# Performance work log

Measured on AMD Instinct MI355X. Metric: run time of the kernel, lower is better.

The kernel has to match this reference:

```python
import jax, jax.numpy as jnp
import numpy as np

B, N_E, E_DIM = 131072, 1024, 64
BETA = 0.25


def setup_inputs() -> dict:
    key = jax.random.key(0)
    kz, kw = jax.random.split(key)
    z = jax.random.normal(kz, (B, E_DIM), dtype=jnp.float32)
    # nn.Embedding init: uniform(-1/n_e, 1/n_e)
    emb_w = jax.random.uniform(kw, (N_E, E_DIM), dtype=jnp.float32,
                               minval=-1.0 / N_E, maxval=1.0 / N_E)
    return {"z": z, "emb_w": emb_w}


def reference(z, emb_w):
    beta = jnp.float32(BETA)
    # pairwise squared distances: [B, n_e]
    d = (jnp.sum(z * z, axis=1, keepdims=True)
         + jnp.sum(emb_w * emb_w, axis=1)
         - 2.0 * jnp.einsum('bd,nd->bn', z, emb_w))
    idx = jnp.argmin(d, axis=1)                      # [B]
    z_q = jnp.take(emb_w, idx, axis=0)               # [B, e_dim]
    # legacy=False branch
    loss = (beta * jnp.mean((jax.lax.stop_gradient(z_q) - z) ** 2)
            + jnp.mean((z_q - jax.lax.stop_gradient(z)) ** 2))
    # straight-through estimator
    z_q_st = z + jax.lax.stop_gradient(z_q - z)
    # torch.var is unbiased (ddof=1)
    v = jnp.var(idx.astype(jnp.float32), ddof=1)
    return (z_q_st, loss, idx, v)
```

## Files before the change

kernel.cpp:

```cpp
#include <hip/hip_runtime.h>
#include <stdint.h>


typedef __attribute__((ext_vector_type(8))) __bf16 bf16x8;
typedef __attribute__((ext_vector_type(4))) float f32x4;

#define OUT_LOSS 8388608
#define OUT_IDX  8388609
#define OUT_VAR  8519681

#define WS_LOSS  0
#define WS_S1    4096
#define WS_S2    8192
#define WS_EFRAG 12288
#define WS_EE    143360

__device__ __forceinline__ void gld_lds16(const void* g, void* l) {
  __builtin_amdgcn_global_load_lds(
      (const __attribute__((address_space(1))) unsigned*)g,
      (__attribute__((address_space(3))) unsigned*)l, 16, 0, 0);
}

__global__ void vq_prep(const float* __restrict__ emb, char* __restrict__ ws) {
  bf16x8* efrag = (bf16x8*)(ws + WS_EFRAG);
  float* eeoff = (float*)(ws + WS_EE);
  const int t = blockIdx.x;
  const int l = threadIdx.x;
  const int n = t * 16 + (l & 15);
  const int kb0 = (l >> 4) * 8;
  const float* er = emb + n * 64;
  for (int j = 0; j < 2; ++j) {
    const int kb = j * 32 + kb0;
    bf16x8 h;
#pragma unroll
    for (int i = 0; i < 8; ++i) h[i] = (__bf16)(-2.0f * er[kb + i]);
    efrag[(t * 2 + j) * 64 + l] = h;
  }
  if (l < 16) {
    const float* e2 = emb + (t * 16 + l) * 64;
    float s = 0.f;
#pragma unroll
    for (int d = 0; d < 64; ++d) s += e2[d] * e2[d];
    eeoff[t * 16 + l] = s + 0.875f;
  }
}

__global__ void __launch_bounds__(512) vq_main(
    const float* __restrict__ z, const float* __restrict__ emb,
    float* __restrict__ out, char* __restrict__ ws) {
  __shared__ char smfrag[3][16384];
  __shared__ float see[1024];
  __shared__ float sL[8];
  __shared__ int sA[8], sB[8];

  const int tid = threadIdx.x;
  const int wave = tid >> 6, lane = tid & 63;
  const int lr = lane & 15, ksl = lane >> 4;
  const int k0 = ksl * 8;
  const int row_base = blockIdx.x * 256 + wave * 32;

#define STAGE(ph, buf)                                                          \
  {                                                                             \
    _Pragma("unroll")                                                           \
    for (int i_ = 0; i_ < 2; ++i_)                                              \
      gld_lds16(ws + WS_EFRAG + (ph) * 16384 + wave * 2048 + i_ * 1024 + lane * 16, \
                smfrag[buf] + wave * 2048 + i_ * 1024);                         \
  }

  const float* zra = z + (size_t)(row_base + lr) * 64;
  const float* zrb = z + (size_t)(row_base + 16 + lr) * 64;
  f32x4 a0 = *(const f32x4*)(zra + k0);
  f32x4 a1 = *(const f32x4*)(zra + k0 + 4);
  f32x4 a2 = *(const f32x4*)(zra + 32 + k0);
  f32x4 a3 = *(const f32x4*)(zra + 32 + k0 + 4);
  f32x4 b0 = *(const f32x4*)(zrb + k0);
  f32x4 b1 = *(const f32x4*)(zrb + k0 + 4);
  f32x4 b2 = *(const f32x4*)(zrb + 32 + k0);
  f32x4 b3 = *(const f32x4*)(zrb + 32 + k0 + 4);

  if (wave < 4)
    gld_lds16(ws + WS_EE + wave * 1024 + lane * 16, (char*)see + wave * 1024);
  STAGE(0, 0);
  STAGE(1, 1);

  bf16x8 zfa0, zfa1, zfb0, zfb1;
  float zza, zzb;
  {
    float sa = 0.f, sb = 0.f;
#pragma unroll
    for (int i = 0; i < 4; ++i) {
      zfa0[i] = (__bf16)a0[i]; zfa0[4 + i] = (__bf16)a1[i];
      zfa1[i] = (__bf16)a2[i]; zfa1[4 + i] = (__bf16)a3[i];
      zfb0[i] = (__bf16)b0[i]; zfb0[4 + i] = (__bf16)b1[i];
      zfb1[i] = (__bf16)b2[i]; zfb1[4 + i] = (__bf16)b3[i];
      sa += a0[i] * a0[i] + a1[i] * a1[i] + a2[i] * a2[i] + a3[i] * a3[i];
      sb += b0[i] * b0[i] + b1[i] * b1[i] + b2[i] * b2[i] + b3[i] * b3[i];
    }
    sa += __shfl_xor(sa, 16, 64); sa += __shfl_xor(sa, 32, 64);
    sb += __shfl_xor(sb, 16, 64); sb += __shfl_xor(sb, 32, 64);
    zza = sa; zzb = sb;
  }

  unsigned rka = 0xFFFFFFFFu, rkb = 0xFFFFFFFFu;
  const unsigned kj0 = (unsigned)(ksl * 4), kj1 = kj0 + 1, kj2 = kj0 + 2, kj3 = kj0 + 3;

  for (int ph = 0; ph < 8; ++ph) {
    if (ph < 7) { asm volatile("s_waitcnt vmcnt(2)" ::: "memory"); }
    else        { asm volatile("s_waitcnt vmcnt(0)" ::: "memory"); }
    __builtin_amdgcn_sched_barrier(0);
    __builtin_amdgcn_s_barrier();
    if (ph < 6) STAGE(ph + 2, (ph + 2) % 3);
    const bf16x8* sfrag = (const bf16x8*)(smfrag[ph % 3]);
    __builtin_amdgcn_s_setprio(1);
#pragma unroll
    for (int tt = 0; tt < 8; ++tt) {
      const int g = ph * 8 + tt;
      bf16x8 e0 = sfrag[(tt * 2 + 0) * 64 + lane];
      bf16x8 e1 = sfrag[(tt * 2 + 1) * 64 + lane];
      const f32x4 ee = *(const f32x4*)(see + g * 16 + ksl * 4);
      f32x4 a = __builtin_amdgcn_mfma_f32_16x16x32_bf16(e0, zfa0, ee, 0, 0, 0);
      a = __builtin_amdgcn_mfma_f32_16x16x32_bf16(e1, zfa1, a, 0, 0, 0);
      f32x4 b = __builtin_amdgcn_mfma_f32_16x16x32_bf16(e0, zfb0, ee, 0, 0, 0);
      b = __builtin_amdgcn_mfma_f32_16x16x32_bf16(e1, zfb1, b, 0, 0, 0);
      const unsigned g16 = (unsigned)(g * 16);
      {
        const unsigned q0 = (__float_as_uint(a[0]) << 10) + kj0;
        const unsigned q1 = (__float_as_uint(a[1]) << 10) + kj1;
        const unsigned q2 = (__float_as_uint(a[2]) << 10) + kj2;
        const unsigned q3 = (__float_as_uint(a[3]) << 10) + kj3;
        rka = min(rka, min(min(q0, q1), min(q2, q3)) + g16);
      }
      {
        const unsigned q0 = (__float_as_uint(b[0]) << 10) + kj0;
        const unsigned q1 = (__float_as_uint(b[1]) << 10) + kj1;
        const unsigned q2 = (__float_as_uint(b[2]) << 10) + kj2;
        const unsigned q3 = (__float_as_uint(b[3]) << 10) + kj3;
        rkb = min(rkb, min(min(q0, q1), min(q2, q3)) + g16);
      }
    }
    __builtin_amdgcn_s_setprio(0);
  }
#undef STAGE

  rka = min(rka, (unsigned)__shfl_xor((int)rka, 16, 64));
  rka = min(rka, (unsigned)__shfl_xor((int)rka, 32, 64));
  rkb = min(rkb, (unsigned)__shfl_xor((int)rkb, 16, 64));
  rkb = min(rkb, (unsigned)__shfl_xor((int)rkb, 32, 64));

  const int erow = lane >> 1, eseg = lane & 1;
  const int src = erow & 15;
  const unsigned ka = (unsigned)__shfl((int)rka, src, 64);
  const unsigned kb = (unsigned)__shfl((int)rkb, src, 64);
  const float za = __shfl(zza, src, 64);
  const float zb = __shfl(zzb, src, 64);
  const unsigned k = (erow < 16) ? ka : kb;
  const float zzv = (erow < 16) ? za : zb;
  const unsigned idx = k & 1023u;
  const size_t rowg = (size_t)row_base + erow;
  const f32x4* ep = (const f32x4*)(emb + (size_t)idx * 64 + eseg * 32);
  f32x4* op = (f32x4*)(out + rowg * 64 + eseg * 32);
#pragma unroll
  for (int c = 0; c < 8; ++c) op[c] = ep[c];

  float ls = 0.f; int s1 = 0, s2 = 0;
  if (eseg == 0) {
    ls = zzv + __uint_as_float(0x3F400000u | (k >> 10)) - 0.875f;
    s1 = (int)idx;
    s2 = (int)(idx * idx);
    out[OUT_IDX + rowg] = (float)idx;
  }
#pragma unroll
  for (int off = 1; off < 64; off <<= 1) {
    ls += __shfl_xor(ls, off, 64);
    s1 += __shfl_xor(s1, off, 64);
    s2 += __shfl_xor(s2, off, 64);
  }
  if (lane == 0) { sL[wave] = ls; sA[wave] = s1; sB[wave] = s2; }
  __syncthreads();
  if (tid == 0) {
    float L = 0; int a = 0, b = 0;
#pragma unroll
    for (int w = 0; w < 8; ++w) { L += sL[w]; a += sA[w]; b += sB[w]; }
    ((float*)(ws + WS_LOSS))[blockIdx.x] = L;
    ((int*)(ws + WS_S1))[blockIdx.x] = a;
    ((int*)(ws + WS_S2))[blockIdx.x] = b;
  }
}

__global__ void vq_final(float* __restrict__ out, const char* __restrict__ ws) {
  const int t = threadIdx.x;
  const float* lp = (const float*)(ws + WS_LOSS);
  const int* p1 = (const int*)(ws + WS_S1);
  const int* p2 = (const int*)(ws + WS_S2);
  double L = 0; long long a = 0, b = 0;
#pragma unroll
  for (int kk = 0; kk < 2; ++kk) {
    const int i = t + 256 * kk;
    L += (double)lp[i];
    a += (long long)p1[i];
    b += (long long)p2[i];
  }
#pragma unroll
  for (int off = 1; off < 64; off <<= 1) {
    L += __shfl_xor(L, off, 64);
    a += __shfl_xor(a, off, 64);
    b += __shfl_xor(b, off, 64);
  }
  __shared__ double sLf[4];
  __shared__ long long sAf[4], sBf[4];
  const int wave = t >> 6, lane = t & 63;
  if (lane == 0) { sLf[wave] = L; sAf[wave] = a; sBf[wave] = b; }
  __syncthreads();
  if (t == 0) {
    double Lt = 0; long long at = 0, bt = 0;
#pragma unroll
    for (int w = 0; w < 4; ++w) { Lt += sLf[w]; at += sAf[w]; bt += sBf[w]; }
    out[OUT_LOSS] = (float)(1.25 * Lt / 8388608.0);
    long long num = bt * 131072LL - at * at;
    out[OUT_VAR] = (float)((double)num / (131072.0 * 131071.0));
  }
}

extern "C" void kernel_launch(void* const* d_in, const int* in_sizes, int n_in,
                              void* d_out, int out_size, void* d_ws, size_t ws_size,
                              hipStream_t stream) {
  (void)in_sizes; (void)n_in; (void)out_size; (void)ws_size;
  const float* z = (const float*)d_in[0];
  const float* emb = (const float*)d_in[1];
  float* out = (float*)d_out;
  char* ws = (char*)d_ws;
  vq_prep<<<64, 64, 0, stream>>>(emb, ws);
  vq_main<<<512, 512, 0, stream>>>(z, emb, out, ws);
  vq_final<<<1, 256, 0, stream>>>(out, ws);
}
```

Baseline: 45.92 us.

## Process 64 rows per wave with 4 waves per block to reuse codebook fragments

Each wave now handles four 16-row z tiles instead of two, and blocks shrink to 256 threads, so each codebook fragment loaded from LDS feeds twice as many MFMAs. LDS fragment loads are batched four tiles ahead of the MFMAs, and the packed distance/index key changes from shift-and-add to mask-and-or with a 0.5 offset. This cuts LDS read traffic per MFMA, at the cost of more registers per lane and half as many waves per block for hiding latency. The masked key drops the low mantissa bits of the distance, which can change tie-breaking.

Result: slower. 48.88 us (+6.4%).

```diff
diff --git a/kernel.cpp b/kernel.cpp
--- a/kernel.cpp
+++ b/kernel.cpp
@@ -41,71 +41,70 @@
     float s = 0.f;
 #pragma unroll
     for (int d = 0; d < 64; ++d) s += e2[d] * e2[d];
-    eeoff[t * 16 + l] = s + 0.875f;
-  }
-}
-
-__global__ void __launch_bounds__(512) vq_main(
+    eeoff[t * 16 + l] = s + 0.5f;
+  }
+}
+
+__global__ void __launch_bounds__(256) vq_main(
     const float* __restrict__ z, const float* __restrict__ emb,
     float* __restrict__ out, char* __restrict__ ws) {
   __shared__ char smfrag[3][16384];
   __shared__ float see[1024];
-  __shared__ float sL[8];
-  __shared__ int sA[8], sB[8];
+  __shared__ float sL[4];
+  __shared__ int sA[4], sB[4];
 
   const int tid = threadIdx.x;
   const int wave = tid >> 6, lane = tid & 63;
   const int lr = lane & 15, ksl = lane >> 4;
   const int k0 = ksl * 8;
-  const int row_base = blockIdx.x * 256 + wave * 32;
+  const int row_base = blockIdx.x * 256 + wave * 64;
 
 #define STAGE(ph, buf)                                                          \
   {                                                                             \
     _Pragma("unroll")                                                           \
-    for (int i_ = 0; i_ < 2; ++i_)                                              \
-      gld_lds16(ws + WS_EFRAG + (ph) * 16384 + wave * 2048 + i_ * 1024 + lane * 16, \
-                smfrag[buf] + wave * 2048 + i_ * 1024);                         \
-  }
-
-  const float* zra = z + (size_t)(row_base + lr) * 64;
-  const float* zrb = z + (size_t)(row_base + 16 + lr) * 64;
-  f32x4 a0 = *(const f32x4*)(zra + k0);
-  f32x4 a1 = *(const f32x4*)(zra + k0 + 4);
-  f32x4 a2 = *(const f32x4*)(zra + 32 + k0);
-  f32x4 a3 = *(const f32x4*)(zra + 32 + k0 + 4);
-  f32x4 b0 = *(const f32x4*)(zrb + k0);
-  f32x4 b1 = *(const f32x4*)(zrb + k0 + 4);
-  f32x4 b2 = *(const f32x4*)(zrb + 32 + k0);
-  f32x4 b3 = *(const f32x4*)(zrb + 32 + k0 + 4);
-
-  if (wave < 4)
-    gld_lds16(ws + WS_EE + wave * 1024 + lane * 16, (char*)see + wave * 1024);
+    for (int i_ = 0; i_ < 4; ++i_)                                              \
+      gld_lds16(ws + WS_EFRAG + (ph) * 16384 + wave * 4096 + i_ * 1024 + lane * 16, \
+                smfrag[buf] + wave * 4096 + i_ * 1024);                         \
+  }
+
+  f32x4 zr[16];
+#pragma unroll
+  for (int r = 0; r < 4; ++r) {
+    const float* zp = z + (size_t)(row_base + r * 16 + lr) * 64;
+    zr[r * 4 + 0] = *(const f32x4*)(zp + k0);
+    zr[r * 4 + 1] = *(const f32x4*)(zp + k0 + 4);
+    zr[r * 4 + 2] = *(const f32x4*)(zp + 32 + k0);
+    zr[r * 4 + 3] = *(const f32x4*)(zp + 32 + k0 + 4);
+  }
+
+  gld_lds16(ws + WS_EE + wave * 1024 + lane * 16, (char*)see + wave * 1024);
   STAGE(0, 0);
   STAGE(1, 1);
 
-  bf16x8 zfa0, zfa1, zfb0, zfb1;
-  float zza, zzb;
-  {
-    float sa = 0.f, sb = 0.f;
+  bf16x8 zf[4][2];
+  float zz[4];
+#pragma unroll
+  for (int r = 0; r < 4; ++r) {
+    float s = 0.f;
 #pragma unroll
     for (int i = 0; i < 4; ++i) {
-      zfa0[i] = (__bf16)a0[i]; zfa0[4 + i] = (__bf16)a1[i];
-      zfa1[i] = (__bf16)a2[i]; zfa1[4 + i] = (__bf16)a3[i];
-      zfb0[i] = (__bf16)b0[i]; zfb0[4 + i] = (__bf16)b1[i];
-      zfb1[i] = (__bf16)b2[i]; zfb1[4 + i] = (__bf16)b3[i];
-      sa += a0[i] * a0[i] + a1[i] * a1[i] + a2[i] * a2[i] + a3[i] * a3[i];
-      sb += b0[i] * b0[i] + b1[i] * b1[i] + b2[i] * b2[i] + b3[i] * b3[i];
+      zf[r][0][i] = (__bf16)zr[r * 4 + 0][i]; zf[r][0][4 + i] = (__bf16)zr[r * 4 + 1][i];
+      zf[r][1][i] = (__bf16)zr[r * 4 + 2][i]; zf[r][1][4 + i] = (__bf16)zr[r * 4 + 3][i];
+      s += zr[r * 4 + 0][i] * zr[r * 4 + 0][i] + zr[r * 4 + 1][i] * zr[r * 4 + 1][i]
+         + zr[r * 4 + 2][i] * zr[r * 4 + 2][i] + zr[r * 4 + 3][i] * zr[r * 4 + 3][i];
     }
-    sa += __shfl_xor(sa, 16, 64); sa += __shfl_xor(sa, 32, 64);
-    sb += __shfl_xor(sb, 16, 64); sb += __shfl_xor(sb, 32, 64);
-    zza = sa; zzb = sb;
-  }
-
-  unsigned rka = 0xFFFFFFFFu, rkb = 0xFFFFFFFFu;
+    s += __shfl_xor(s, 16, 64);
+    s += __shfl_xor(s, 32, 64);
+    zz[r] = s;
+  }
+
+  unsigned rk[4];
+#pragma unroll
+  for (int r = 0; r < 4; ++r) rk[r] = 0xFFFFFFFFu;
   const unsigned kj0 = (unsigned)(ksl * 4), kj1 = kj0 + 1, kj2 = kj0 + 2, kj3 = kj0 + 3;
 
   for (int ph = 0; ph < 8; ++ph) {
-    if (ph < 7) { asm volatile("s_waitcnt vmcnt(2)" ::: "memory"); }
+    if (ph < 7) { asm volatile("s_waitcnt vmcnt(4)" ::: "memory"); }
     else        { asm volatile("s_waitcnt vmcnt(0)" ::: "memory"); }
     __builtin_amdgcn_sched_barrier(0);
     __builtin_amdgcn_s_barrier();
@@ -113,61 +112,66 @@
     const bf16x8* sfrag = (const bf16x8*)(smfrag[ph % 3]);
     __builtin_amdgcn_s_setprio(1);
 #pragma unroll
-    for (int tt = 0; tt < 8; ++tt) {
-      const int g = ph * 8 + tt;
-      bf16x8 e0 = sfrag[(tt * 2 + 0) * 64 + lane];
-      bf16x8 e1 = sfrag[(tt * 2 + 1) * 64 + lane];
-      const f32x4 ee = *(const f32x4*)(see + g * 16 + ksl * 4);
-      f32x4 a = __builtin_amdgcn_mfma_f32_16x16x32_bf16(e0, zfa0, ee, 0, 0, 0);
-      a = __builtin_amdgcn_mfma_f32_16x16x32_bf16(e1, zfa1, a, 0, 0, 0);
-      f32x4 b = __builtin_amdgcn_mfma_f32_16x16x32_bf16(e0, zfb0, ee, 0, 0, 0);
-      b = __builtin_amdgcn_mfma_f32_16x16x32_bf16(e1, zfb1, b, 0, 0, 0);
-      const unsigned g16 = (unsigned)(g * 16);
-      {
-        const unsigned q0 = (__float_as_uint(a[0]) << 10) + kj0;
-        const unsigned q1 = (__float_as_uint(a[1]) << 10) + kj1;
-        const unsigned q2 = (__float_as_uint(a[2]) << 10) + kj2;
-        const unsigned q3 = (__float_as_uint(a[3]) << 10) + kj3;
-        rka = min(rka, min(min(q0, q1), min(q2, q3)) + g16);
+    for (int half = 0; half < 2; ++half) {
+      bf16x8 E0[4], E1[4];
+      f32x4 EE[4];
+#pragma unroll
+      for (int q = 0; q < 4; ++q) {
+        const int tt = half * 4 + q;
+        E0[q] = sfrag[(tt * 2 + 0) * 64 + lane];
+        E1[q] = sfrag[(tt * 2 + 1) * 64 + lane];
+        EE[q] = *(const f32x4*)(see + (ph * 8 + tt) * 16 + ksl * 4);
       }
-      {
-        const unsigned q0 = (__float_as_uint(b[0]) << 10) + kj0;
-        const unsigned q1 = (__float_as_uint(b[1]) << 10) + kj1;
-        const unsigned q2 = (__float_as_uint(b[2]) << 10) + kj2;
-        const unsigned q3 = (__float_as_uint(b[3]) << 10) + kj3;
-        rkb = min(rkb, min(min(q0, q1), min(q2, q3)) + g16);
+#pragma unroll
+      for (int q = 0; q < 4; ++q) {
+        const unsigned g16 = (unsigned)((ph * 8 + half * 4 + q) * 16);
+#pragma unroll
+        for (int r = 0; r < 4; ++r) {
+          f32x4 a = __builtin_amdgcn_mfma_f32_16x16x32_bf16(E0[q], zf[r][0], EE[q], 0, 0, 0);
+          a = __builtin_amdgcn_mfma_f32_16x16x32_bf16(E1[q], zf[r][1], a, 0, 0, 0);
+          const unsigned t0 = (__float_as_uint(a[0]) & 0xFFFFFC00u) | kj0;
+          const unsigned t1 = (__float_as_uint(a[1]) & 0xFFFFFC00u) | kj1;
+          const unsigned t2 = (__float_as_uint(a[2]) & 0xFFFFFC00u) | kj2;
+          const unsigned t3 = (__float_as_uint(a[3]) & 0xFFFFFC00u) | kj3;
+          const unsigned m = min(min(min(t0, t1), t2), t3);
+          rk[r] = min(rk[r], m + g16);
+        }
       }
     }
     __builtin_amdgcn_s_setprio(0);
   }
 #undef STAGE
 
-  rka = min(rka, (unsigned)__shfl_xor((int)rka, 16, 64));
-  rka = min(rka, (unsigned)__shfl_xor((int)rka, 32, 64));
-  rkb = min(rkb, (unsigned)__shfl_xor((int)rkb, 16, 64));
-  rkb = min(rkb, (unsigned)__shfl_xor((int)rkb, 32, 64));
-
+#pragma unroll
+  for (int r = 0; r < 4; ++r) {
+    rk[r] = min(rk[r], (unsigned)__shfl_xor((int)rk[r], 16, 64));
+    rk[r] = min(rk[r], (unsigned)__shfl_xor((int)rk[r], 32, 64));
+  }
+
+  float ls = 0.f; int s1 = 0, s2 = 0;
   const int erow = lane >> 1, eseg = lane & 1;
   const int src = erow & 15;
-  const unsigned ka = (unsigned)__shfl((int)rka, src, 64);
-  const unsigned kb = (unsigned)__shfl((int)rkb, src, 64);
-  const float za = __shfl(zza, src, 64);
-  const float zb = __shfl(zzb, src, 64);
-  const unsigned k = (erow < 16) ? ka : kb;
-  const float zzv = (erow < 16) ? za : zb;
-  const unsigned idx = k & 1023u;
-  const size_t rowg = (size_t)row_base + erow;
-  const f32x4* ep = (const f32x4*)(emb + (size_t)idx * 64 + eseg * 32);
-  f32x4* op = (f32x4*)(out + rowg * 64 + eseg * 32);
-#pragma unroll
-  for (int c = 0; c < 8; ++c) op[c] = ep[c];
-
-  float ls = 0.f; int s1 = 0, s2 = 0;
-  if (eseg == 0) {
-    ls = zzv + __uint_as_float(0x3F400000u | (k >> 10)) - 0.875f;
-    s1 = (int)idx;
-    s2 = (int)(idx * idx);
-    out[OUT_IDX + rowg] = (float)idx;
+  const int hi = erow >> 4;
+#pragma unroll
+  for (int h = 0; h < 2; ++h) {
+    const unsigned ka = (unsigned)__shfl((int)rk[h * 2 + 0], src, 64);
+    const unsigned kb = (unsigned)__shfl((int)rk[h * 2 + 1], src, 64);
+    const float za = __shfl(zz[h * 2 + 0], src, 64);
+    const float zb = __shfl(zz[h * 2 + 1], src, 64);
+    const unsigned k = hi ? kb : ka;
+    const float zzv = hi ? zb : za;
+    const unsigned idx = k & 1023u;
+    const size_t rowg = (size_t)row_base + h * 32 + erow;
+    const f32x4* ep = (const f32x4*)(emb + (size_t)idx * 64 + eseg * 32);
+    f32x4* op = (f32x4*)(out + rowg * 64 + eseg * 32);
+#pragma unroll
+    for (int c = 0; c < 8; ++c) op[c] = ep[c];
+    if (eseg == 0) {
+      ls += zzv + __uint_as_float(k & 0xFFFFFC00u) - 0.5f;
+      s1 += (int)idx;
+      s2 += (int)(idx * idx);
+      out[OUT_IDX + rowg] = (float)idx;
+    }
   }
 #pragma unroll
   for (int off = 1; off < 64; off <<= 1) {
@@ -180,7 +184,7 @@
   if (tid == 0) {
     float L = 0; int a = 0, b = 0;
 #pragma unroll
-    for (int w = 0; w < 8; ++w) { L += sL[w]; a += sA[w]; b += sB[w]; }
+    for (int w = 0; w < 4; ++w) { L += sL[w]; a += sA[w]; b += sB[w]; }
     ((float*)(ws + WS_LOSS))[blockIdx.x] = L;
     ((int*)(ws + WS_S1))[blockIdx.x] = a;
     ((int*)(ws + WS_S2))[blockIdx.x] = b;
@@ -230,6 +234,6 @@
   float* out = (float*)d_out;
   char* ws = (char*)d_ws;
   vq_prep<<<64, 64, 0, stream>>>(emb, ws);
-  vq_main<<<512, 512, 0, stream>>>(z, emb, out, ws);
+  vq_main<<<512, 256, 0, stream>>>(z, emb, out, ws);
   vq_final<<<1, 256, 0, stream>>>(out, ws);
 }
```
